# Optimization experiments

Measured on AMD Instinct MI355X. Metric: run time of the kernel, lower is better.

Reference implementation:

```python
import jax, jax.numpy as jnp
import numpy as np

N = 50000          # num nodes
E = 800000         # num edges (before self loops)
IN_C = 128
HID = 256          # heads * head_dim
HEADS = 4
HEAD_DIM = HID // HEADS
OUT_C = 64
NEG_SLOPE = 0.2    # PyG GATConv default leaky_relu slope
BN_EPS = 1e-5


def _gat_conv(x, src, dst, W, att_src, att_dst, bias, concat):
    """PyG-style GATConv (with self loops already appended to src/dst).
    x: [N, in_c]; W: [in_c, H*C]; att_src/att_dst: [H, C]; bias: [H*C] or [C]."""
    H, C = att_src.shape
    h = (x @ W).reshape(-1, H, C)                               # [N, H, C]
    a_src = jnp.einsum('nhc,hc->nh', h, att_src)                # [N, H]
    a_dst = jnp.einsum('nhc,hc->nh', h, att_dst)                # [N, H]
    e = jax.nn.leaky_relu(a_src[src] + a_dst[dst], NEG_SLOPE)   # [Et, H]
    # segment softmax over destination nodes (numerically stable)
    m = jax.ops.segment_max(e, dst, num_segments=N)             # [N, H]
    m = jnp.where(jnp.isfinite(m), m, 0.0)
    ex = jnp.exp(e - m[dst])
    denom = jax.ops.segment_sum(ex, dst, num_segments=N)        # [N, H]
    alpha = ex / (denom[dst] + 1e-16)                           # [Et, H]
    msg = alpha[:, :, None] * h[src]                            # [Et, H, C]
    out = jax.ops.segment_sum(msg, dst, num_segments=N)         # [N, H, C]
    out = out.reshape(N, H * C) if concat else out.mean(axis=1)
    return out + bias


def _bn_eval(x, gamma, beta, mean, var):
    return (x - mean) * jax.lax.rsqrt(var + BN_EPS) * gamma + beta


def setup_inputs() -> dict:
    key = jax.random.key(0)
    ks = jax.random.split(key, 16)
    x = jax.random.normal(ks[0], (N, IN_C), dtype=jnp.float32)
    edge_index = jax.random.randint(ks[1], (2, E), 0, N, dtype=jnp.int64)

    def lin(k, fan_in, fan_out):
        s = (1.0 / np.sqrt(fan_in)).astype(np.float32)
        return jax.random.normal(k, (fan_in, fan_out), dtype=jnp.float32) * s

    def att(k, h, c):
        return jax.random.normal(k, (h, c), dtype=jnp.float32) * 0.1

    return {
        'x': x, 'edge_index': edge_index,
        'W0': lin(ks[2], IN_C, HID), 'as0': att(ks[3], HEADS, HEAD_DIM), 'ad0': att(ks[4], HEADS, HEAD_DIM), 'b0': jnp.zeros((HID,), jnp.float32),
        'bn0_g': jnp.ones((HID,), jnp.float32), 'bn0_b': jnp.zeros((HID,), jnp.float32), 'bn0_m': jnp.zeros((HID,), jnp.float32), 'bn0_v': jnp.ones((HID,), jnp.float32),
        'W1': lin(ks[5], HID, HID), 'as1': att(ks[6], HEADS, HEAD_DIM), 'ad1': att(ks[7], HEADS, HEAD_DIM), 'b1': jnp.zeros((HID,), jnp.float32),
        'bn1_g': jnp.ones((HID,), jnp.float32), 'bn1_b': jnp.zeros((HID,), jnp.float32), 'bn1_m': jnp.zeros((HID,), jnp.float32), 'bn1_v': jnp.ones((HID,), jnp.float32),
        'W2': lin(ks[8], HID, OUT_C), 'as2': att(ks[9], 1, OUT_C), 'ad2': att(ks[10], 1, OUT_C), 'b2': jnp.zeros((OUT_C,), jnp.float32),
    }


def reference(x, edge_index, W0, as0, ad0, b0, bn0_g, bn0_b, bn0_m, bn0_v,
              W1, as1, ad1, b1, bn1_g, bn1_b, bn1_m, bn1_v,
              W2, as2, ad2, b2):
    loop = jnp.arange(N, dtype=edge_index.dtype)
    src = jnp.concatenate([edge_index[0], loop])   # PyG add_self_loops=True
    dst = jnp.concatenate([edge_index[1], loop])

    h = _gat_conv(x, src, dst, W0, as0, ad0, b0, concat=True)
    h = jax.nn.elu(_bn_eval(h, bn0_g, bn0_b, bn0_m, bn0_v))   # dropout: eval -> identity
    h = _gat_conv(h, src, dst, W1, as1, ad1, b1, concat=True)
    h = jax.nn.elu(_bn_eval(h, bn1_g, bn1_b, bn1_m, bn1_v))
    out = _gat_conv(h, src, dst, W2, as2, ad2, b2, concat=False)  # heads=1, mean
    return out
```

## Files before the change

### kernel.cpp

```cpp
#include <hip/hip_runtime.h>

#define NN   50000
#define EE   800000
#define ET   850000
#define INC  128
#define HID  256
#define OUTC 64
#define NEG  0.2f
#define BNEPS 1e-5f

typedef __bf16 bf16x8 __attribute__((ext_vector_type(8)));
typedef float  f32x4  __attribute__((ext_vector_type(4)));

static __device__ __forceinline__ float b2f(unsigned short u) {
    return __uint_as_float(((unsigned)u) << 16);
}
static __device__ __forceinline__ float blo(unsigned u) {
    return __uint_as_float(u << 16);
}
static __device__ __forceinline__ float bhi(unsigned u) {
    return __uint_as_float(u & 0xFFFF0000u);
}
static __device__ __forceinline__ unsigned short f2b(float f) {
    unsigned u = __float_as_uint(f);
    unsigned r = u + 0x7FFFu + ((u >> 16) & 1u);
    return (unsigned short)(r >> 16);
}
static __device__ __forceinline__ float leaky(float x) {
    return x > 0.f ? x : NEG * x;
}
static __device__ __forceinline__ float ew(float e) {
    return __expf(fminf(e, 80.f));
}

__global__ void k_init(const int* __restrict__ ei, const unsigned* __restrict__ xw,
                       int* __restrict__ cnt, int* __restrict__ flagW, int* __restrict__ flagB,
                       int nbZ) {
    __shared__ int cs[4];
    int b = blockIdx.x, t = threadIdx.x;
    if (b < nbZ) {
        int i = b * 256 + t;
        if (i < NN) cnt[i] = 0;
    } else if (b == nbZ) {
        int c = 0;
        for (int k = 0; k < 16; k++) {
            int i = t + 256 * k;
            if (ei[2 * i + 1] != 0) c = 1;
        }
        for (int o = 1; o < 64; o <<= 1) c |= __shfl_xor(c, o);
        if ((t & 63) == 0) cs[t >> 6] = c;
        __syncthreads();
        if (t == 0) *flagW = cs[0] | cs[1] | cs[2] | cs[3];
    } else {
        int c = 0;
        for (int i = t; i < 4096; i += 256) {
            unsigned v = (xw[i] >> 8) & 0x7F;
            if (v >= 50 && v <= 67) c++;
        }
        for (int o = 1; o < 64; o <<= 1) c += __shfl_xor(c, o);
        if ((t & 63) == 0) cs[t >> 6] = c;
        __syncthreads();
        if (t == 0) *flagB = (cs[0] + cs[1] + cs[2] + cs[3] > 2048) ? 1 : 0;
    }
}

static __device__ __forceinline__ void hist_body(int b, const int* __restrict__ ei,
                                                 const int* __restrict__ flagW,
                                                 int* __restrict__ cnt) {
    int j = b * 256 + threadIdx.x;
    int i0 = 2 * j;
    if (i0 >= ET) return;
    int d0, d1;
    if (i0 < EE) {
        if (*flagW) {
            uint2 dv = *(const uint2*)(ei + EE + i0);
            d0 = dv.x; d1 = dv.y;
        } else {
            uint4 dv = *(const uint4*)(ei + 2 * (EE + i0));
            d0 = dv.x; d1 = dv.z;
        }
    } else {
        d0 = i0 - EE; d1 = i0 + 1 - EE;
    }
    atomicAdd(&cnt[d0], 1);
    atomicAdd(&cnt[d1], 1);
}

static __device__ void prep_body(int b,
                       const void* as0, const void* ad0, const void* b0, const void* g0,
                       const void* be0, const void* m0, const void* v0,
                       const void* as1, const void* ad1, const void* b1, const void* g1,
                       const void* be1, const void* m1, const void* v1,
                       const void* as2, const void* ad2, const void* b2,
                       const void* W0, const void* W1, const void* W2,
                       unsigned short* __restrict__ WT0, unsigned short* __restrict__ WT1,
                       unsigned short* __restrict__ WT2,
                       const void* __restrict__ x, unsigned short* __restrict__ xb,
                       float* __restrict__ pp, const int* __restrict__ flagB) {
    int t = threadIdx.x;
    bool bf = (*flagB != 0);
    auto cv = [&](const void* s, int i) -> float {
        return bf ? b2f(((const unsigned short*)s)[i]) : ((const float*)s)[i];
    };
    if (b < 14) {
        float v;
        switch (b) {
            case 0:  v = cv(as0, t); break;
            case 1:  v = cv(ad0, t); break;
            case 2:  v = cv(b0, t);  break;
            case 3:  v = cv(g0, t);  break;
            case 4:  v = cv(be0, t); break;
            case 5:  v = cv(m0, t);  break;
            case 6:  v = cv(v0, t);  break;
            case 7:  v = cv(as1, t); break;
            case 8:  v = cv(ad1, t); break;
            case 9:  v = cv(b1, t);  break;
            case 10: v = cv(g1, t);  break;
            case 11: v = cv(be1, t); break;
            case 12: v = cv(m1, t);  break;
            default: v = cv(v1, t);  break;
        }
        pp[b * 256 + t] = v;
    } else if (b == 14) {
        if (t < 192) {
            int arr = t >> 6, j = t & 63;
            float v = (arr == 0) ? cv(as2, j) : (arr == 1) ? cv(ad2, j) : cv(b2, j);
            pp[14 * 256 + arr * 64 + j] = v;
        }
    } else if (b < 15 + 128) {
        int i = (b - 15) * 256 + t;
        int k = i >> 8, n = i & 255;
        WT0[n * INC + k] = bf ? ((const unsigned short*)W0)[i] : f2b(((const float*)W0)[i]);
    } else if (b < 15 + 128 + 256) {
        int i = (b - 143) * 256 + t;
        int k = i >> 8, n = i & 255;
        WT1[n * HID + k] = bf ? ((const unsigned short*)W1)[i] : f2b(((const float*)W1)[i]);
    } else if (b < 15 + 128 + 256 + 64) {
        int i = (b - 399) * 256 + t;
        int k = i >> 6, n = i & 63;
        WT2[n * HID + k] = bf ? ((const unsigned short*)W2)[i] : f2b(((const float*)W2)[i]);
    } else {
        if (bf) return;
        for (int i = (b - 463) * 256 + t; i < NN * INC; i += 2048 * 256)
            xb[i] = f2b(((const float*)x)[i]);
    }
}

#define NB_HIST 1661
__global__ __launch_bounds__(256) void k_histprep(
                       const int* __restrict__ ei, const int* __restrict__ flagW,
                       int* __restrict__ cnt,
                       const void* as0, const void* ad0, const void* b0, const void* g0,
                       const void* be0, const void* m0, const void* v0,
                       const void* as1, const void* ad1, const void* b1, const void* g1,
                       const void* be1, const void* m1, const void* v1,
                       const void* as2, const void* ad2, const void* b2,
                       const void* W0, const void* W1, const void* W2,
                       unsigned short* __restrict__ WT0, unsigned short* __restrict__ WT1,
                       unsigned short* __restrict__ WT2,
                       const void* __restrict__ x, unsigned short* __restrict__ xb,
                       float* __restrict__ pp, const int* __restrict__ flagB) {
    int b = blockIdx.x;
    if (b < NB_HIST) hist_body(b, ei, flagW, cnt);
    else prep_body(b - NB_HIST, as0, ad0, b0, g0, be0, m0, v0,
                   as1, ad1, b1, g1, be1, m1, v1, as2, ad2, b2,
                   W0, W1, W2, WT0, WT1, WT2, x, xb, pp, flagB);
}

static __device__ __forceinline__ int block_scan_incl(int v, int t, int* ws) {
    int lane = t & 63, w = t >> 6;
    int x = v;
    for (int o = 1; o < 64; o <<= 1) {
        int y = __shfl_up(x, o);
        if (lane >= o) x += y;
    }
    if (lane == 63) ws[w] = x;
    __syncthreads();
    if (t == 0) {
        int s = 0;
        for (int k = 0; k < 4; k++) { int tmp = ws[k]; ws[k] = s; s += tmp; }
    }
    __syncthreads();
    return x + ws[w];
}

__global__ void k_scan_a(const int* __restrict__ cnt, int* __restrict__ rowptr, int* __restrict__ bsum) {
    __shared__ int ws[4];
    int t = threadIdx.x, b = blockIdx.x;
    int i = b * 256 + t;
    int v = (i < NN) ? cnt[i] : 0;
    int incl = block_scan_incl(v, t, ws);
    if (i < NN) rowptr[i] = incl - v;
    if (t == 255) bsum[b] = incl;
}

__global__ void k_scan_b(int* __restrict__ bsum, int nb) {
    __shared__ int ws[4];
    int t = threadIdx.x;
    int v = (t < nb) ? bsum[t] : 0;
    int incl = block_scan_incl(v, t, ws);
    if (t < nb) bsum[t] = incl - v;
}

__global__ void k_scan_c(int* __restrict__ rowptr, const int* __restrict__ bsum, int* __restrict__ cursor) {
    int t = threadIdx.x, b = blockIdx.x;
    int i = b * 256 + t;
    if (i < NN) {
        int r = rowptr[i] + bsum[b];
        rowptr[i] = r;
        cursor[i] = r;
    }
    if (i == 0) rowptr[NN] = ET;
}

static __device__ __forceinline__ void scatter_body(int b, const int* __restrict__ ei,
                                                    const int* __restrict__ flagW,
                                                    int* __restrict__ cursor,
                                                    int* __restrict__ esrc) {
    int j = b * 256 + threadIdx.x;
    int i0 = 2 * j;
    if (i0 >= ET + 64) return;
    if (i0 >= ET) {
        esrc[i0] = 0;
        if (i0 + 1 < ET + 64) esrc[i0 + 1] = 0;
        return;
    }
    int s0, d0, s1, d1;
    if (i0 < EE) {
        if (*flagW) {
            uint2 sv = *(const uint2*)(ei + i0);
            uint2 dv = *(const uint2*)(ei + EE + i0);
            s0 = sv.x; s1 = sv.y; d0 = dv.x; d1 = dv.y;
        } else {
            uint4 sv = *(const uint4*)(ei + 2 * i0);
            uint4 dv = *(const uint4*)(ei + 2 * (EE + i0));
            s0 = sv.x; s1 = sv.z; d0 = dv.x; d1 = dv.z;
        }
    } else {
        s0 = d0 = i0 - EE; s1 = d1 = i0 + 1 - EE;
    }
    int p0 = atomicAdd(&cursor[d0], 1); esrc[p0] = s0;
    int p1 = atomicAdd(&cursor[d1], 1); esrc[p1] = s1;
}

template<int NC, int NH, int NBN>
static __device__ void gemm_body(int bm, int bg, const unsigned short* __restrict__ A,
                                 const unsigned short* __restrict__ WT,
                                 unsigned short* __restrict__ H,
                                 float* __restrict__ asrc, float* __restrict__ adst,
                                 const float* __restrict__ asv, const float* __restrict__ adv,
                                 int M, int K) {
    constexpr int BN = 64 * NBN;
    __shared__ __align__(16) unsigned short As[128 * 40];
    __shared__ __align__(16) unsigned short Bs[BN * 40];
    int t = threadIdx.x;
    int lane = t & 63, wave = t >> 6;
    int m16 = lane & 15, quad = lane >> 4;

    f32x4 acc[2][4 * NBN];
    #pragma unroll
    for (int a = 0; a < 2; a++)
        #pragma unroll
        for (int b = 0; b < 4 * NBN; b++) acc[a][b] = (f32x4){0.f, 0.f, 0.f, 0.f};

    int arow = t >> 1, ahalf = t & 1;
    long gArow = (long)bm * 128 + arow;

    for (int k0 = 0; k0 < K; k0 += 32) {
        uint4 av0 = {0u, 0u, 0u, 0u}, av1 = {0u, 0u, 0u, 0u};
        if (gArow < M) {
            const unsigned short* ap = A + gArow * (size_t)K + k0 + ahalf * 16;
            av0 = *(const uint4*)(ap);
            av1 = *(const uint4*)(ap + 8);
        }
        if constexpr (NBN == 2) {
            const unsigned short* bp = WT + ((size_t)bg * BN + arow) * K + k0 + ahalf * 16;
            uint4 bv0 = *(const uint4*)(bp);
            uint4 bv1 = *(const uint4*)(bp + 8);
            *(uint4*)&As[arow * 40 + ahalf * 16]     = av0;
            *(uint4*)&As[arow * 40 + ahalf * 16 + 8] = av1;
            *(uint4*)&Bs[arow * 40 + ahalf * 16]     = bv0;
            *(uint4*)&Bs[arow * 40 + ahalf * 16 + 8] = bv1;
        } else {
            int brow = t >> 2, bq = t & 3;
            uint4 bv = *(const uint4*)(WT + ((size_t)bg * BN + brow) * K + k0 + bq * 8);
            *(uint4*)&As[arow * 40 + ahalf * 16]     = av0;
            *(uint4*)&As[arow * 40 + ahalf * 16 + 8] = av1;
            *(uint4*)&Bs[brow * 40 + bq * 8]         = bv;
        }
        __syncthreads();
        int wrow = wave * 32;
        bf16x8 af[2], bf[4 * NBN];
        #pragma unroll
        for (int mt = 0; mt < 2; mt++)
            af[mt] = *(const bf16x8*)&As[(wrow + mt * 16 + m16) * 40 + quad * 8];
        #pragma unroll
        for (int nt = 0; nt < 4 * NBN; nt++)
            bf[nt] = *(const bf16x8*)&Bs[(nt * 16 + m16) * 40 + quad * 8];
        #pragma unroll
        for (int mt = 0; mt < 2; mt++)
            #pragma unroll
            for (int nt = 0; nt < 4 * NBN; nt++)
                acc[mt][nt] = __builtin_amdgcn_mfma_f32_16x16x32_bf16(af[mt], bf[nt], acc[mt][nt], 0, 0, 0);
        __syncthreads();
    }

    float asc[4 * NBN], adc[4 * NBN];
    #pragma unroll
    for (int nt = 0; nt < 4 * NBN; nt++) {
        int col = bg * BN + nt * 16 + m16;
        asc[nt] = asv[col];
        adc[nt] = adv[col];
    }
    #pragma unroll
    for (int mt = 0; mt < 2; mt++) {
        int gR0 = bm * 128 + wave * 32 + mt * 16 + quad * 4;
        #pragma unroll
        for (int r = 0; r < 4; r++) {
            int gR = gR0 + r;
            #pragma unroll
            for (int hh = 0; hh < NBN; hh++) {
                float ps = 0.f, pd = 0.f;
                #pragma unroll
                for (int nt = hh * 4; nt < hh * 4 + 4; nt++) {
                    float v = acc[mt][nt][r];
                    ps += v * asc[nt];
                    pd += v * adc[nt];
                }
                for (int o = 1; o < 16; o <<= 1) { ps += __shfl_xor(ps, o); pd += __shfl_xor(pd, o); }
                if (m16 == 0 && gR < M) {
                    asrc[(size_t)gR * NH + bg * NBN + hh] = ps;
                    adst[(size_t)gR * NH + bg * NBN + hh] = pd;
                }
            }
            if (gR < M) {
                #pragma unroll
                for (int nt = 0; nt < 4 * NBN; nt++) {
                    int gC = bg * BN + nt * 16 + m16;
                    H[(size_t)gR * NC + gC] = f2b(acc[mt][nt][r]);
                }
            }
        }
    }
}

template<int NC, int NH, int NBN>
__global__ __launch_bounds__(256) void k_gemm(const unsigned short* __restrict__ Amain,
                                              const void* __restrict__ Aalt,
                                              const int* __restrict__ flagB,
                                              const unsigned short* __restrict__ WT,
                                              unsigned short* __restrict__ H,
                                              float* __restrict__ asrc, float* __restrict__ adst,
                                              const float* __restrict__ asv, const float* __restrict__ adv,
                                              int M, int K) {
    const unsigned short* A = (*flagB) ? (const unsigned short*)Aalt : Amain;
    gemm_body<NC, NH, NBN>(blockIdx.x, blockIdx.y, A, WT, H, asrc, adst, asv, adv, M, K);
}

#define NB_G0 (((NN + 127) / 128) * 2)
__global__ __launch_bounds__(256) void k_scatgemm0(
        const int* __restrict__ ei, const int* __restrict__ flagW,
        int* __restrict__ cursor, int* __restrict__ esrc,
        const unsigned short* __restrict__ Amain, const void* __restrict__ Aalt,
        const int* __restrict__ flagB, const unsigned short* __restrict__ WT,
        unsigned short* __restrict__ H, float* __restrict__ asrc, float* __restrict__ adst,
        const float* __restrict__ asv, const float* __restrict__ adv) {
    int b = blockIdx.x;
    if (b < NB_G0) {
        const unsigned short* A = (*flagB) ? (const unsigned short*)Aalt : Amain;
        gemm_body<HID, 4, 2>(b >> 1, b & 1, A, WT, H, asrc, adst, asv, adv, NN, INC);
    } else {
        scatter_body(b - NB_G0, ei, flagW, cursor, esrc);
    }
}

#define LOADG(pre, d, e0n) \
    uint2 pre##0 = {0, 0}, pre##1 = {0, 0}, pre##2 = {0, 0}, pre##3 = {0, 0}; \
    if (d) { \
        int s0_ = esrc[(e0n)], s1_ = esrc[(e0n) + 1], s2_ = esrc[(e0n) + 2], s3_ = esrc[(e0n) + 3]; \
        pre##0 = *(const uint2*)(h + (size_t)s0_ * HID + lc); \
        pre##1 = *(const uint2*)(h + (size_t)s1_ * HID + lc); \
        pre##2 = *(const uint2*)(h + (size_t)s2_ * HID + lc); \
        pre##3 = *(const uint2*)(h + (size_t)s3_ * HID + lc); \
    }
#define FMAG(pre, d, wreg, A0, A1, A2, A3, j) \
    if (d) { \
        float w0_ = __shfl(wreg, wsel + (j)),     w1_ = __shfl(wreg, wsel + (j) + 1); \
        float w2_ = __shfl(wreg, wsel + (j) + 2), w3_ = __shfl(wreg, wsel + (j) + 3); \
        A0 += w0_ * blo((pre##0).x) + w1_ * blo((pre##1).x) + w2_ * blo((pre##2).x) + w3_ * blo((pre##3).x); \
        A1 += w0_ * bhi((pre##0).x) + w1_ * bhi((pre##1).x) + w2_ * bhi((pre##2).x) + w3_ * bhi((pre##3).x); \
        A2 += w0_ * blo((pre##0).y) + w1_ * blo((pre##1).y) + w2_ * blo((pre##2).y) + w3_ * blo((pre##3).y); \
        A3 += w0_ * bhi((pre##0).y) + w1_ * bhi((pre##1).y) + w2_ * bhi((pre##2).y) + w3_ * bhi((pre##3).y); \
    }

__global__ __launch_bounds__(256, 4) void k_agg4(const unsigned short* __restrict__ h,
                       const float* __restrict__ asrc, const float* __restrict__ adst,
                       const int* __restrict__ rowptr, const int* __restrict__ esrc,
                       const float* __restrict__ bias,
                       const float* __restrict__ bng, const float* __restrict__ bnb,
                       const float* __restrict__ bnm, const float* __restrict__ bnv,
                       unsigned short* __restrict__ act) {
    int t = threadIdx.x;
    int wave = t >> 6, lane = t & 63;
    int nodeA = blockIdx.x * 8 + wave * 2;
    if (nodeA >= NN) return;
    int nodeB = nodeA + 1;
    bool hasB = (nodeB < NN);

    int hd = lane >> 4, li = lane & 15;
    int wsel = lane & 48;
    const size_t lc = (size_t)lane * 4;

    int e0A = __builtin_amdgcn_readfirstlane(rowptr[nodeA]);
    int e1A = __builtin_amdgcn_readfirstlane(rowptr[nodeA + 1]);
    int degA = e1A - e0A;
    int e0B = e1A, degB = 0;
    if (hasB) degB = __builtin_amdgcn_readfirstlane(rowptr[nodeB + 1]) - e1A;

    float adhA = adst[(size_t)nodeA * 4 + hd];
    float adhB = hasB ? adst[(size_t)nodeB * 4 + hd] : 0.f;

    float waccA = 0.f, waccB = 0.f;
    float aA0 = 0.f, aA1 = 0.f, aA2 = 0.f, aA3 = 0.f;
    float aB0 = 0.f, aB1 = 0.f, aB2 = 0.f, aB3 = 0.f;

    int nA = min(16, degA), nB = min(16, degB);
    float eA = 0.f, eB = 0.f;
    if (li < nA) { int s = esrc[e0A + li]; eA = asrc[(size_t)s * 4 + hd]; }
    if (li < nB) { int s = esrc[e0B + li]; eB = asrc[(size_t)s * 4 + hd]; }

    int degM = max(degA, degB);
    for (int c = 0; c < degM; c += 16) {
        float wA = (li < nA) ? ew(leaky(eA + adhA)) : 0.f;
        float wB = (li < nB) ? ew(leaky(eB + adhB)) : 0.f;
        waccA += wA; waccB += wB;
        int nA2 = min(16, degA - (c + 16));
        int nB2 = min(16, degB - (c + 16));
        eA = 0.f; eB = 0.f;
        if (li < nA2) { int s = esrc[e0A + c + 16 + li]; eA = asrc[(size_t)s * 4 + hd]; }
        if (li < nB2) { int s = esrc[e0B + c + 16 + li]; eB = asrc[(size_t)s * 4 + hd]; }
        bool dA0 = 0 < nA, dA1 = 4 < nA, dA2 = 8 < nA, dA3 = 12 < nA;
        bool dB0 = 0 < nB, dB1 = 4 < nB, dB2 = 8 < nB, dB3 = 12 < nB;
        LOADG(gA0, dA0, e0A + c)
        LOADG(gA1, dA1, e0A + c + 4)
        LOADG(gA2, dA2, e0A + c + 8)
        LOADG(gA3, dA3, e0A + c + 12)
        LOADG(gB0, dB0, e0B + c)
        LOADG(gB1, dB1, e0B + c + 4)
        LOADG(gB2, dB2, e0B + c + 8)
        LOADG(gB3, dB3, e0B + c + 12)
        FMAG(gA0, dA0, wA, aA0, aA1, aA2, aA3, 0)
        FMAG(gA1, dA1, wA, aA0, aA1, aA2, aA3, 4)
        FMAG(gA2, dA2, wA, aA0, aA1, aA2, aA3, 8)
        FMAG(gA3, dA3, wA, aA0, aA1, aA2, aA3, 12)
        FMAG(gB0, dB0, wB, aB0, aB1, aB2, aB3, 0)
        FMAG(gB1, dB1, wB, aB0, aB1, aB2, aB3, 4)
        FMAG(gB2, dB2, wB, aB0, aB1, aB2, aB3, 8)
        FMAG(gB3, dB3, wB, aB0, aB1, aB2, aB3, 12)
        nA = nA2; nB = nB2;
    }
    waccA += __shfl_xor(waccA, 1); waccA += __shfl_xor(waccA, 2);
    waccA += __shfl_xor(waccA, 4); waccA += __shfl_xor(waccA, 8);
    waccB += __shfl_xor(waccB, 1); waccB += __shfl_xor(waccB, 2);
    waccB += __shfl_xor(waccB, 4); waccB += __shfl_xor(waccB, 8);
    float invA = 1.f / (waccA + 1e-16f);
    float invB = 1.f / (waccB + 1e-16f);

    int c0 = lane * 4;
    float4 bi = *(const float4*)(bias + c0);
    float4 bm_ = *(const float4*)(bnm + c0);
    float4 bv_ = *(const float4*)(bnv + c0);
    float4 bg_ = *(const float4*)(bng + c0);
    float4 bb_ = *(const float4*)(bnb + c0);
    float sc[4], sh[4];
    {
        const float* bvp = (const float*)&bv_;
        const float* bgp = (const float*)&bg_;
        const float* bmp = (const float*)&bm_;
        const float* bbp = (const float*)&bb_;
        const float* bip = (const float*)&bi;
        #pragma unroll
        for (int jj = 0; jj < 4; jj++) {
            float s_ = rsqrtf(bvp[jj] + BNEPS) * bgp[jj];
            sc[jj] = s_;
            sh[jj] = bbp[jj] + (bip[jj] - bmp[jj]) * s_;
        }
    }
    {
        float o[4] = {aA0 * invA, aA1 * invA, aA2 * invA, aA3 * invA};
        unsigned short res[4];
        #pragma unroll
        for (int jj = 0; jj < 4; jj++) {
            float val = o[jj] * sc[jj] + sh[jj];
            val = val > 0.f ? val : expm1f(val);
            res[jj] = f2b(val);
        }
        *(ushort4*)(act + (size_t)nodeA * HID + c0) = *(ushort4*)res;
    }
    if (hasB) {
        float o[4] = {aB0 * invB, aB1 * invB, aB2 * invB, aB3 * invB};
        unsigned short res[4];
        #pragma unroll
        for (int jj = 0; jj < 4; jj++) {
            float val = o[jj] * sc[jj] + sh[jj];
            val = val > 0.f ? val : expm1f(val);
            res[jj] = f2b(val);
        }
        *(ushort4*)(act + (size_t)nodeB * HID + c0) = *(ushort4*)res;
    }
}

__global__ void k_agg1(const unsigned short* __restrict__ h,
                       const float* __restrict__ asrc, const float* __restrict__ adst,
                       const int* __restrict__ rowptr, const int* __restrict__ esrc,
                       const float* __restrict__ bias,
                       void* __restrict__ outp, const int* __restrict__ flagB) {
    int t = threadIdx.x;
    int wave = t >> 6, lane = t & 63;
    int node0 = blockIdx.x * 16 + wave * 4;
    int q = lane >> 4, lq = lane & 15;
    int qs = lane & 48;
    int node = node0 + q;
    const size_t lc4 = (size_t)lq * 4;

    int e0  = rowptr[node];
    int deg = rowptr[node + 1] - e0;
    float ad = adst[node];

    float den = 0.f;
    float a0 = 0.f, a1 = 0.f, a2 = 0.f, a3 = 0.f;

    int n = min(16, deg);
    int s = 0; float e = 0.f;
    if (lq < n) { s = esrc[e0 + lq]; e = asrc[s]; }

    int degM = deg;
    degM = max(degM, __shfl_xor(degM, 16));
    degM = max(degM, __shfl_xor(degM, 32));

    for (int c = 0; c < degM; c += 16) {
        float w = (lq < n) ? ew(leaky(e + ad)) : 0.f;
        den += w;
        int n2 = min(16, deg - (c + 16));
        int sN = 0; float eN = 0.f;
        if (lq < n2) { sN = esrc[e0 + c + 16 + lq]; eN = asrc[sN]; }
        #pragma unroll
        for (int g = 0; g < 4; g++) {
            int j = g * 4;
            if (j < n) {
                int s0 = __shfl(s, qs + j),     s1 = __shfl(s, qs + j + 1);
                int s2 = __shfl(s, qs + j + 2), s3 = __shfl(s, qs + j + 3);
                float w0 = __shfl(w, qs + j),     w1 = __shfl(w, qs + j + 1);
                float w2 = __shfl(w, qs + j + 2), w3 = __shfl(w, qs + j + 3);
                uint2 v0 = *(const uint2*)(h + (size_t)s0 * OUTC + lc4);
                uint2 v1 = *(const uint2*)(h + (size_t)s1 * OUTC + lc4);
                uint2 v2 = *(const uint2*)(h + (size_t)s2 * OUTC + lc4);
                uint2 v3 = *(const uint2*)(h + (size_t)s3 * OUTC + lc4);
                a0 += w0 * blo(v0.x) + w1 * blo(v1.x) + w2 * blo(v2.x) + w3 * blo(v3.x);
                a1 += w0 * bhi(v0.x) + w1 * bhi(v1.x) + w2 * bhi(v2.x) + w3 * bhi(v3.x);
                a2 += w0 * blo(v0.y) + w1 * blo(v1.y) + w2 * blo(v2.y) + w3 * blo(v3.y);
                a3 += w0 * bhi(v0.y) + w1 * bhi(v1.y) + w2 * bhi(v2.y) + w3 * bhi(v3.y);
            }
        }
        s = sN; e = eN; n = n2;
    }
    den += __shfl_xor(den, 1); den += __shfl_xor(den, 2);
    den += __shfl_xor(den, 4); den += __shfl_xor(den, 8);
    float inv = 1.f / (den + 1e-16f);
    int c0 = lq * 4;
    float v0 = a0 * inv + bias[c0];
    float v1 = a1 * inv + bias[c0 + 1];
    float v2 = a2 * inv + bias[c0 + 2];
    float v3 = a3 * inv + bias[c0 + 3];
    if (*flagB) {
        unsigned r0 = (unsigned)f2b(v0) | ((unsigned)f2b(v1) << 16);
        unsigned r1 = (unsigned)f2b(v2) | ((unsigned)f2b(v3) << 16);
        uint2 rv = {r0, r1};
        *(uint2*)((unsigned short*)outp + (size_t)node * OUTC + c0) = rv;
    } else {
        float4 rv = {v0, v1, v2, v3};
        *(float4*)((float*)outp + (size_t)node * OUTC + c0) = rv;
    }
}

extern "C" void kernel_launch(void* const* d_in, const int* in_sizes, int n_in,
                              void* d_out, int out_size, void* d_ws, size_t ws_size,
                              hipStream_t stream) {
    const void* x  = d_in[0];
    const int*  ei = (const int*)d_in[1];
    const void* W0 = d_in[2];
    const void* W1 = d_in[10];
    const void* W2 = d_in[18];

    char* ws = (char*)d_ws;
    size_t off = 0;
    auto alloc = [&](size_t n) { void* p = ws + off; off += (n + 255) & ~(size_t)255; return p; };

    unsigned short* xb  = (unsigned short*)alloc((size_t)NN * INC * 2);
    unsigned short* h   = (unsigned short*)alloc((size_t)NN * HID * 2);
    unsigned short* act = (unsigned short*)alloc((size_t)NN * HID * 2);
    unsigned short* WT0 = (unsigned short*)alloc((size_t)HID * INC * 2);
    unsigned short* WT1 = (unsigned short*)alloc((size_t)HID * HID * 2);
    unsigned short* WT2 = (unsigned short*)alloc((size_t)OUTC * HID * 2);
    float*          pp  = (float*)alloc((size_t)(14 * 256 + 3 * 64) * 4);
    float*  asrc   = (float*)alloc((size_t)NN * 4 * 4);
    float*  adst   = (float*)alloc((size_t)NN * 4 * 4);
    int*    cnt    = (int*)alloc((size_t)(NN + 2) * 4);
    int*    rowptr = (int*)alloc((size_t)(NN + 1) * 4);
    int*    cursor = (int*)alloc((size_t)NN * 4);
    int*    esrc   = (int*)alloc((size_t)(ET + 64) * 4);
    int*    bsum   = (int*)alloc(256 * 4);
    int*    flagW  = cnt + NN;
    int*    flagB  = cnt + NN + 1;

    float* P0 = pp;
    float* P1 = pp + 7 * 256;
    float* P2 = pp + 14 * 256;

    const int nbN = (NN + 255) / 256;
    const int nbHP = NB_HIST + 463 + 2048;
    const int nbSG = NB_G0 + 1661;
    const int nbA4 = (NN + 7) / 8;
    const int nbA1 = NN / 16;
    dim3 gemmGrid1((NN + 127) / 128, HID / 128);
    dim3 gemmGrid2((NN + 127) / 128, 1);

    k_init<<<nbN + 2, 256, 0, stream>>>(ei, (const unsigned*)x, cnt, flagW, flagB, nbN);
    k_histprep<<<nbHP, 256, 0, stream>>>(ei, flagW, cnt,
                                         d_in[3], d_in[4], d_in[5], d_in[6], d_in[7], d_in[8], d_in[9],
                                         d_in[11], d_in[12], d_in[13], d_in[14], d_in[15], d_in[16], d_in[17],
                                         d_in[19], d_in[20], d_in[21],
                                         W0, W1, W2, WT0, WT1, WT2, x, xb, pp, flagB);
    k_scan_a<<<nbN, 256, 0, stream>>>(cnt, rowptr, bsum);
    k_scan_b<<<1, 256, 0, stream>>>(bsum, nbN);
    k_scan_c<<<nbN, 256, 0, stream>>>(rowptr, bsum, cursor);
    k_scatgemm0<<<nbSG, 256, 0, stream>>>(ei, flagW, cursor, esrc,
                                          xb, x, flagB, WT0, h, asrc, adst,
                                          P0 + 0, P0 + 256);
    k_agg4<<<nbA4, 256, 0, stream>>>(h, asrc, adst, rowptr, esrc,
                                     P0 + 512, P0 + 768, P0 + 1024, P0 + 1280, P0 + 1536, act);
    k_gemm<HID, 4, 2><<<gemmGrid1, 256, 0, stream>>>(act, act, flagB, WT1, h, asrc, adst,
                                                     P1 + 0, P1 + 256, NN, HID);
    k_agg4<<<nbA4, 256, 0, stream>>>(h, asrc, adst, rowptr, esrc,
                                     P1 + 512, P1 + 768, P1 + 1024, P1 + 1280, P1 + 1536, act);
    k_gemm<OUTC, 1, 1><<<gemmGrid2, 256, 0, stream>>>(act, act, flagB, WT2, h, asrc, adst,
                                                      P2 + 0, P2 + 64, NN, HID);
    k_agg1<<<nbA1, 256, 0, stream>>>(h, asrc, adst, rowptr, esrc, P2 + 128, d_out, flagB);
}
```

Measured before the change: 445.3 us.

## Split agg4 work across column slices per block and unfuse scatter/gemm0

Rewrites the 4-head aggregation so each block handles 16 nodes for one 32-column slice (8 slices per node group), with each 16-lane quarter-wave owning one node and half-quarters splitting the edges. Source indices and weights are broadcast by shuffle instead of being reloaded per lane. This is meant to raise parallelism and cut per-wave register pressure, in exchange for recomputing the attention softmax denominator in every slice. The fused scatter+gemm0 kernel is also split back into separate scatter and gemm launches, which adds a launch and loses their overlap. The new grid assumes NN is a multiple of 16.

```diff
diff --git a/kernel.cpp b/kernel.cpp
--- a/kernel.cpp
+++ b/kernel.cpp
@@ -213,11 +213,9 @@
     if (i == 0) rowptr[NN] = ET;
 }
 
-static __device__ __forceinline__ void scatter_body(int b, const int* __restrict__ ei,
-                                                    const int* __restrict__ flagW,
-                                                    int* __restrict__ cursor,
-                                                    int* __restrict__ esrc) {
-    int j = b * 256 + threadIdx.x;
+__global__ void k_scatter(const int* __restrict__ ei, const int* __restrict__ flagW,
+                          int* __restrict__ cursor, int* __restrict__ esrc) {
+    int j = blockIdx.x * 256 + threadIdx.x;
     int i0 = 2 * j;
     if (i0 >= ET + 64) return;
     if (i0 >= ET) {
@@ -244,16 +242,20 @@
 }
 
 template<int NC, int NH, int NBN>
-static __device__ void gemm_body(int bm, int bg, const unsigned short* __restrict__ A,
-                                 const unsigned short* __restrict__ WT,
-                                 unsigned short* __restrict__ H,
-                                 float* __restrict__ asrc, float* __restrict__ adst,
-                                 const float* __restrict__ asv, const float* __restrict__ adv,
-                                 int M, int K) {
+__global__ __launch_bounds__(256) void k_gemm(const unsigned short* __restrict__ Amain,
+                                              const void* __restrict__ Aalt,
+                                              const int* __restrict__ flagB,
+                                              const unsigned short* __restrict__ WT,
+                                              unsigned short* __restrict__ H,
+                                              float* __restrict__ asrc, float* __restrict__ adst,
+                                              const float* __restrict__ asv, const float* __restrict__ adv,
+                                              int M, int K) {
     constexpr int BN = 64 * NBN;
     __shared__ __align__(16) unsigned short As[128 * 40];
     __shared__ __align__(16) unsigned short Bs[BN * 40];
+    const unsigned short* A = (*flagB) ? (const unsigned short*)Aalt : Amain;
     int t = threadIdx.x;
+    int bm = blockIdx.x, bg = blockIdx.y;
     int lane = t & 63, wave = t >> 6;
     int m16 = lane & 15, quad = lane >> 4;
 
@@ -344,55 +346,6 @@
     }
 }
 
-template<int NC, int NH, int NBN>
-__global__ __launch_bounds__(256) void k_gemm(const unsigned short* __restrict__ Amain,
-                                              const void* __restrict__ Aalt,
-                                              const int* __restrict__ flagB,
-                                              const unsigned short* __restrict__ WT,
-                                              unsigned short* __restrict__ H,
-                                              float* __restrict__ asrc, float* __restrict__ adst,
-                                              const float* __restrict__ asv, const float* __restrict__ adv,
-                                              int M, int K) {
-    const unsigned short* A = (*flagB) ? (const unsigned short*)Aalt : Amain;
-    gemm_body<NC, NH, NBN>(blockIdx.x, blockIdx.y, A, WT, H, asrc, adst, asv, adv, M, K);
-}
-
-#define NB_G0 (((NN + 127) / 128) * 2)
-__global__ __launch_bounds__(256) void k_scatgemm0(
-        const int* __restrict__ ei, const int* __restrict__ flagW,
-        int* __restrict__ cursor, int* __restrict__ esrc,
-        const unsigned short* __restrict__ Amain, const void* __restrict__ Aalt,
-        const int* __restrict__ flagB, const unsigned short* __restrict__ WT,
-        unsigned short* __restrict__ H, float* __restrict__ asrc, float* __restrict__ adst,
-        const float* __restrict__ asv, const float* __restrict__ adv) {
-    int b = blockIdx.x;
-    if (b < NB_G0) {
-        const unsigned short* A = (*flagB) ? (const unsigned short*)Aalt : Amain;
-        gemm_body<HID, 4, 2>(b >> 1, b & 1, A, WT, H, asrc, adst, asv, adv, NN, INC);
-    } else {
-        scatter_body(b - NB_G0, ei, flagW, cursor, esrc);
-    }
-}
-
-#define LOADG(pre, d, e0n) \
-    uint2 pre##0 = {0, 0}, pre##1 = {0, 0}, pre##2 = {0, 0}, pre##3 = {0, 0}; \
-    if (d) { \
-        int s0_ = esrc[(e0n)], s1_ = esrc[(e0n) + 1], s2_ = esrc[(e0n) + 2], s3_ = esrc[(e0n) + 3]; \
-        pre##0 = *(const uint2*)(h + (size_t)s0_ * HID + lc); \
-        pre##1 = *(const uint2*)(h + (size_t)s1_ * HID + lc); \
-        pre##2 = *(const uint2*)(h + (size_t)s2_ * HID + lc); \
-        pre##3 = *(const uint2*)(h + (size_t)s3_ * HID + lc); \
-    }
-#define FMAG(pre, d, wreg, A0, A1, A2, A3, j) \
-    if (d) { \
-        float w0_ = __shfl(wreg, wsel + (j)),     w1_ = __shfl(wreg, wsel + (j) + 1); \
-        float w2_ = __shfl(wreg, wsel + (j) + 2), w3_ = __shfl(wreg, wsel + (j) + 3); \
-        A0 += w0_ * blo((pre##0).x) + w1_ * blo((pre##1).x) + w2_ * blo((pre##2).x) + w3_ * blo((pre##3).x); \
-        A1 += w0_ * bhi((pre##0).x) + w1_ * bhi((pre##1).x) + w2_ * bhi((pre##2).x) + w3_ * bhi((pre##3).x); \
-        A2 += w0_ * blo((pre##0).y) + w1_ * blo((pre##1).y) + w2_ * blo((pre##2).y) + w3_ * blo((pre##3).y); \
-        A3 += w0_ * bhi((pre##0).y) + w1_ * bhi((pre##1).y) + w2_ * bhi((pre##2).y) + w3_ * bhi((pre##3).y); \
-    }
-
 __global__ __launch_bounds__(256, 4) void k_agg4(const unsigned short* __restrict__ h,
                        const float* __restrict__ asrc, const float* __restrict__ adst,
                        const int* __restrict__ rowptr, const int* __restrict__ esrc,
@@ -402,111 +355,89 @@
                        unsigned short* __restrict__ act) {
     int t = threadIdx.x;
     int wave = t >> 6, lane = t & 63;
-    int nodeA = blockIdx.x * 8 + wave * 2;
-    if (nodeA >= NN) return;
-    int nodeB = nodeA + 1;
-    bool hasB = (nodeB < NN);
-
-    int hd = lane >> 4, li = lane & 15;
-    int wsel = lane & 48;
-    const size_t lc = (size_t)lane * 4;
-
-    int e0A = __builtin_amdgcn_readfirstlane(rowptr[nodeA]);
-    int e1A = __builtin_amdgcn_readfirstlane(rowptr[nodeA + 1]);
-    int degA = e1A - e0A;
-    int e0B = e1A, degB = 0;
-    if (hasB) degB = __builtin_amdgcn_readfirstlane(rowptr[nodeB + 1]) - e1A;
-
-    float adhA = adst[(size_t)nodeA * 4 + hd];
-    float adhB = hasB ? adst[(size_t)nodeB * 4 + hd] : 0.f;
-
-    float waccA = 0.f, waccB = 0.f;
-    float aA0 = 0.f, aA1 = 0.f, aA2 = 0.f, aA3 = 0.f;
-    float aB0 = 0.f, aB1 = 0.f, aB2 = 0.f, aB3 = 0.f;
-
-    int nA = min(16, degA), nB = min(16, degB);
-    float eA = 0.f, eB = 0.f;
-    if (li < nA) { int s = esrc[e0A + li]; eA = asrc[(size_t)s * 4 + hd]; }
-    if (li < nB) { int s = esrc[e0B + li]; eB = asrc[(size_t)s * 4 + hd]; }
-
-    int degM = max(degA, degB);
+    int slice = blockIdx.x & 7;
+    int nblk  = blockIdx.x >> 3;
+    int node0 = nblk * 16 + wave * 4;
+    int q = lane >> 4, lq = lane & 15;
+    int hd = slice >> 1;
+    int coff = slice * 32;
+
+    int prev = __builtin_amdgcn_readfirstlane(rowptr[node0]);
+    int e00, e01, e02, e03, dg0, dg1, dg2, dg3;
+    {
+        int n1 = __builtin_amdgcn_readfirstlane(rowptr[node0 + 1]);
+        int n2 = __builtin_amdgcn_readfirstlane(rowptr[node0 + 2]);
+        int n3 = __builtin_amdgcn_readfirstlane(rowptr[node0 + 3]);
+        int n4 = __builtin_amdgcn_readfirstlane(rowptr[node0 + 4]);
+        e00 = prev; dg0 = n1 - prev;
+        e01 = n1;   dg1 = n2 - n1;
+        e02 = n2;   dg2 = n3 - n2;
+        e03 = n3;   dg3 = n4 - n3;
+    }
+    int e0q = (q == 0) ? e00 : (q == 1) ? e01 : (q == 2) ? e02 : e03;
+    int dgq = (q == 0) ? dg0 : (q == 1) ? dg1 : (q == 2) ? dg2 : dg3;
+    int node = node0 + q;
+    float adh = adst[(size_t)node * 4 + hd];
+
+    float den = 0.f;
+    float a0 = 0.f, a1 = 0.f, a2 = 0.f, a3 = 0.f;
+
+    int nq = min(16, dgq);
+    int s_reg = 0; float e_reg = 0.f;
+    if (lq < nq) { s_reg = esrc[e0q + lq]; e_reg = asrc[(size_t)s_reg * 4 + hd]; }
+
+    int degM = max(max(dg0, dg1), max(dg2, dg3));
+    int esel = (lane & 48) + ((lane >> 3) & 1);
+    const size_t lc = (size_t)(coff + (lane & 7) * 4);
+
     for (int c = 0; c < degM; c += 16) {
-        float wA = (li < nA) ? ew(leaky(eA + adhA)) : 0.f;
-        float wB = (li < nB) ? ew(leaky(eB + adhB)) : 0.f;
-        waccA += wA; waccB += wB;
-        int nA2 = min(16, degA - (c + 16));
-        int nB2 = min(16, degB - (c + 16));
-        eA = 0.f; eB = 0.f;
-        if (li < nA2) { int s = esrc[e0A + c + 16 + li]; eA = asrc[(size_t)s * 4 + hd]; }
-        if (li < nB2) { int s = esrc[e0B + c + 16 + li]; eB = asrc[(size_t)s * 4 + hd]; }
-        bool dA0 = 0 < nA, dA1 = 4 < nA, dA2 = 8 < nA, dA3 = 12 < nA;
-        bool dB0 = 0 < nB, dB1 = 4 < nB, dB2 = 8 < nB, dB3 = 12 < nB;
-        LOADG(gA0, dA0, e0A + c)
-        LOADG(gA1, dA1, e0A + c + 4)
-        LOADG(gA2, dA2, e0A + c + 8)
-        LOADG(gA3, dA3, e0A + c + 12)
-        LOADG(gB0, dB0, e0B + c)
-        LOADG(gB1, dB1, e0B + c + 4)
-        LOADG(gB2, dB2, e0B + c + 8)
-        LOADG(gB3, dB3, e0B + c + 12)
-        FMAG(gA0, dA0, wA, aA0, aA1, aA2, aA3, 0)
-        FMAG(gA1, dA1, wA, aA0, aA1, aA2, aA3, 4)
-        FMAG(gA2, dA2, wA, aA0, aA1, aA2, aA3, 8)
-        FMAG(gA3, dA3, wA, aA0, aA1, aA2, aA3, 12)
-        FMAG(gB0, dB0, wB, aB0, aB1, aB2, aB3, 0)
-        FMAG(gB1, dB1, wB, aB0, aB1, aB2, aB3, 4)
-        FMAG(gB2, dB2, wB, aB0, aB1, aB2, aB3, 8)
-        FMAG(gB3, dB3, wB, aB0, aB1, aB2, aB3, 12)
-        nA = nA2; nB = nB2;
-    }
-    waccA += __shfl_xor(waccA, 1); waccA += __shfl_xor(waccA, 2);
-    waccA += __shfl_xor(waccA, 4); waccA += __shfl_xor(waccA, 8);
-    waccB += __shfl_xor(waccB, 1); waccB += __shfl_xor(waccB, 2);
-    waccB += __shfl_xor(waccB, 4); waccB += __shfl_xor(waccB, 8);
-    float invA = 1.f / (waccA + 1e-16f);
-    float invB = 1.f / (waccB + 1e-16f);
-
-    int c0 = lane * 4;
-    float4 bi = *(const float4*)(bias + c0);
-    float4 bm_ = *(const float4*)(bnm + c0);
-    float4 bv_ = *(const float4*)(bnv + c0);
-    float4 bg_ = *(const float4*)(bng + c0);
-    float4 bb_ = *(const float4*)(bnb + c0);
-    float sc[4], sh[4];
-    {
+        float w = (lq < nq) ? ew(leaky(e_reg + adh)) : 0.f;
+        den += w;
+        int nq2 = min(16, dgq - (c + 16));
+        int s_next = 0; e_reg = 0.f;
+        if (lq < nq2) { s_next = esrc[e0q + c + 16 + lq]; e_reg = asrc[(size_t)s_next * 4 + hd]; }
+        #pragma unroll
+        for (int g = 0; g < 8; g++) {
+            if (2 * g < nq) {
+                int src  = __shfl(s_reg, esel + 2 * g);
+                float wv = __shfl(w,     esel + 2 * g);
+                uint2 hv = *(const uint2*)(h + (size_t)src * HID + lc);
+                a0 += wv * blo(hv.x);
+                a1 += wv * bhi(hv.x);
+                a2 += wv * blo(hv.y);
+                a3 += wv * bhi(hv.y);
+            }
+        }
+        s_reg = s_next; nq = nq2;
+    }
+    a0 += __shfl_xor(a0, 8); a1 += __shfl_xor(a1, 8);
+    a2 += __shfl_xor(a2, 8); a3 += __shfl_xor(a3, 8);
+    den += __shfl_xor(den, 1); den += __shfl_xor(den, 2);
+    den += __shfl_xor(den, 4); den += __shfl_xor(den, 8);
+    float inv = 1.f / (den + 1e-16f);
+
+    if (lq < 8) {
+        int cc = coff + lq * 4;
+        float4 bi  = *(const float4*)(bias + cc);
+        float4 bm_ = *(const float4*)(bnm + cc);
+        float4 bv_ = *(const float4*)(bnv + cc);
+        float4 bg_ = *(const float4*)(bng + cc);
+        float4 bb_ = *(const float4*)(bnb + cc);
+        float o[4] = {a0 * inv, a1 * inv, a2 * inv, a3 * inv};
+        const float* bip = (const float*)&bi;
+        const float* bmp = (const float*)&bm_;
         const float* bvp = (const float*)&bv_;
         const float* bgp = (const float*)&bg_;
-        const float* bmp = (const float*)&bm_;
         const float* bbp = (const float*)&bb_;
-        const float* bip = (const float*)&bi;
+        unsigned short res[4];
         #pragma unroll
         for (int jj = 0; jj < 4; jj++) {
             float s_ = rsqrtf(bvp[jj] + BNEPS) * bgp[jj];
-            sc[jj] = s_;
-            sh[jj] = bbp[jj] + (bip[jj] - bmp[jj]) * s_;
-        }
-    }
-    {
-        float o[4] = {aA0 * invA, aA1 * invA, aA2 * invA, aA3 * invA};
-        unsigned short res[4];
-        #pragma unroll
-        for (int jj = 0; jj < 4; jj++) {
-            float val = o[jj] * sc[jj] + sh[jj];
+            float val = (o[jj] + bip[jj] - bmp[jj]) * s_ + bbp[jj];
             val = val > 0.f ? val : expm1f(val);
             res[jj] = f2b(val);
         }
-        *(ushort4*)(act + (size_t)nodeA * HID + c0) = *(ushort4*)res;
-    }
-    if (hasB) {
-        float o[4] = {aB0 * invB, aB1 * invB, aB2 * invB, aB3 * invB};
-        unsigned short res[4];
-        #pragma unroll
-        for (int jj = 0; jj < 4; jj++) {
-            float val = o[jj] * sc[jj] + sh[jj];
-            val = val > 0.f ? val : expm1f(val);
-            res[jj] = f2b(val);
-        }
-        *(ushort4*)(act + (size_t)nodeB * HID + c0) = *(ushort4*)res;
+        *(ushort4*)(act + (size_t)node * HID + cc) = *(ushort4*)res;
     }
 }
 
@@ -619,9 +550,10 @@
 
     const int nbN = (NN + 255) / 256;
     const int nbHP = NB_HIST + 463 + 2048;
-    const int nbSG = NB_G0 + 1661;
-    const int nbA4 = (NN + 7) / 8;
+    const int nbSc = 1661;
+    const int nbA4 = (NN / 16) * 8;
     const int nbA1 = NN / 16;
+    dim3 gemmGrid0((NN + 127) / 128, HID / 128);
     dim3 gemmGrid1((NN + 127) / 128, HID / 128);
     dim3 gemmGrid2((NN + 127) / 128, 1);
 
@@ -634,9 +566,10 @@
     k_scan_a<<<nbN, 256, 0, stream>>>(cnt, rowptr, bsum);
     k_scan_b<<<1, 256, 0, stream>>>(bsum, nbN);
     k_scan_c<<<nbN, 256, 0, stream>>>(rowptr, bsum, cursor);
-    k_scatgemm0<<<nbSG, 256, 0, stream>>>(ei, flagW, cursor, esrc,
-                                          xb, x, flagB, WT0, h, asrc, adst,
-                                          P0 + 0, P0 + 256);
+    k_scatter<<<nbSc, 256, 0, stream>>>(ei, flagW, cursor, esrc);
+
+    k_gemm<HID, 4, 2><<<gemmGrid0, 256, 0, stream>>>(xb, x, flagB, WT0, h, asrc, adst,
+                                                     P0 + 0, P0 + 256, NN, INC);
     k_agg4<<<nbA4, 256, 0, stream>>>(h, asrc, adst, rowptr, esrc,
                                      P0 + 512, P0 + 768, P0 + 1024, P0 + 1280, P0 + 1536, act);
     k_gemm<HID, 4, 2><<<gemmGrid1, 256, 0, stream>>>(act, act, flagB, WT1, h, asrc, adst,
```

New measurement: 524.7 us. 17.8% more time.
